# Kernel optimization log

Measured on AMD Instinct MI355X. Metric: run time of the kernel, lower is better.

## Reference

```python
import jax, jax.numpy as jnp
import numpy as np

TOP_K = 2
TEMPERATURE = 1.0


def setup_inputs() -> dict:
    key = jax.random.key(0)
    k1, k2, k3 = jax.random.split(key, 3)
    x = jax.random.normal(k1, (4, 2048, 2048), jnp.float32)
    # prototypes are top right-singular vectors of lora_A -> unit norm rows
    protos = jax.random.normal(k2, (8, 2048), jnp.float32)
    protos = protos / jnp.linalg.norm(protos, axis=-1, keepdims=True)
    # precomputed_W = stack of B @ A per expert, shape (E, out, in)
    W = jax.random.normal(k3, (8, 2048, 2048), jnp.float32) * 0.02
    return {"x": x, "prototypes": protos, "W": W, "scaling": 2}


def reference(x, prototypes, W, scaling):
    F_in = x.shape[-1]
    tok = x.reshape(-1, F_in)                      # (t, F)
    t = tok.shape[0]
    E = prototypes.shape[0]
    # Arrow routing: |<tok, proto_e>| similarity, keep top-k, softmax
    sim = jnp.abs(tok @ prototypes.T)              # (t, E)
    top_v, idx = jax.lax.top_k(sim, TOP_K)         # (t, k)
    neg_inf = jnp.asarray(-jnp.inf, tok.dtype)
    full_score = jnp.full((t, E), neg_inf, dtype=tok.dtype)
    full_score = full_score.at[jnp.arange(t)[:, None], idx].set(top_v)
    coeff = jax.nn.softmax(full_score / TEMPERATURE, axis=1)  # (t, E), zero off top-k
    # dense per-expert LoRA delta, then coefficient combine (as in source)
    W_tok = jnp.einsum('eoi,ti->eto', W, tok)      # (E, t, out)
    delta = jnp.einsum('te,eto->to', coeff, W_tok) # (t, out)
    delta = jnp.asarray(scaling, delta.dtype) * delta  # dropout = identity (eval)
    return delta.reshape(*x.shape[:-1], delta.shape[-1])
```

## Files before the change

kernel.cpp:

```cpp
#include <hip/hip_runtime.h>

#define T_TOK 8192
#define F_IN  2048
#define F_OUT 2048
#define N_EXP 8
#define NKS   (F_IN / 64)
#define MAXTILES 144
#define RT_TPB 16

typedef __attribute__((ext_vector_type(8))) short    short8;
typedef __attribute__((ext_vector_type(4))) float    f32x4;
typedef __attribute__((ext_vector_type(8))) _Float16 half8;
typedef unsigned short ushort;

#define AS1 __attribute__((address_space(1)))
#define AS3 __attribute__((address_space(3)))
#define GLOAD16(g, l) __builtin_amdgcn_global_load_lds((const AS1 unsigned int*)(g), \
                                                       (AS3 unsigned int*)(l), 16, 0, 0)

__device__ inline ushort f2bf(float f) {
    unsigned u = __float_as_uint(f);
    u += 0x7FFFu + ((u >> 16) & 1u);
    return (ushort)(u >> 16);
}

__global__ __launch_bounds__(256) void cvt_kernel(const float* __restrict__ in,
                                                  ushort* __restrict__ out, int n8) {
    for (int i = blockIdx.x * 256 + threadIdx.x; i < n8; i += gridDim.x * 256) {
        const float4 a = ((const float4*)in)[i * 2 + 0];
        const float4 b = ((const float4*)in)[i * 2 + 1];
        uint4 v;
        v.x = f2bf(a.x) | ((unsigned)f2bf(a.y) << 16);
        v.y = f2bf(a.z) | ((unsigned)f2bf(a.w) << 16);
        v.z = f2bf(b.x) | ((unsigned)f2bf(b.y) << 16);
        v.w = f2bf(b.z) | ((unsigned)f2bf(b.w) << 16);
        ((uint4*)out)[i] = v;
    }
}

__device__ inline void top2_store(const float* s, int ti, float sc,
                                  int* sh_ei, float (*sh_cf)[2]) {
    float v0 = -1.f; int i0 = 0;
    #pragma unroll
    for (int e = 0; e < N_EXP; ++e) {
        const float a = fabsf(s[e]);
        if (a > v0) { v0 = a; i0 = e; }
    }
    float v1 = -1.f; int i1 = 0;
    #pragma unroll
    for (int e = 0; e < N_EXP; ++e) {
        const float a = fabsf(s[e]);
        if (e != i0 && a > v1) { v1 = a; i1 = e; }
    }
    const float ex  = expf(v1 - v0);
    const float inv = 1.f / (1.f + ex);
    sh_ei[ti]    = i0 | (i1 << 16);
    sh_cf[ti][0] = sc * inv;
    sh_cf[ti][1] = sc * ex * inv;
}

__global__ __launch_bounds__(256) void route_kernel(
    const float* __restrict__ x, const float* __restrict__ protos,
    const int* __restrict__ scaling, ushort* __restrict__ xb,
    int* __restrict__ counts, int* __restrict__ lists, float* __restrict__ coeffs,
    int* __restrict__ pos)
{
    __shared__ int   sh_ei[RT_TPB];
    __shared__ float sh_cf[RT_TPB][2];
    __shared__ int   sh_base[N_EXP];

    const int wave = threadIdx.x >> 6;
    const int lane = threadIdx.x & 63;
    const float sc = (float)(*scaling);

    for (int pr = 0; pr < 2; ++pr) {
        const int ti0  = wave * 4 + pr * 2;
        const int tok0 = blockIdx.x * RT_TPB + ti0;
        const float* xr0 = x  + (size_t)tok0 * F_IN;
        const float* xr1 = xr0 + F_IN;
        ushort*      xo0 = xb + (size_t)tok0 * F_IN;
        ushort*      xo1 = xo0 + F_IN;

        float s0[N_EXP] = {}, s1[N_EXP] = {};
        for (int c = 0; c < F_IN / 256; ++c) {
            const int off = c * 256 + lane * 4;
            const float4 a = *(const float4*)(xr0 + off);
            const float4 b = *(const float4*)(xr1 + off);
            uint2 ba, bb;
            ba.x = f2bf(a.x) | ((unsigned)f2bf(a.y) << 16);
            ba.y = f2bf(a.z) | ((unsigned)f2bf(a.w) << 16);
            bb.x = f2bf(b.x) | ((unsigned)f2bf(b.y) << 16);
            bb.y = f2bf(b.z) | ((unsigned)f2bf(b.w) << 16);
            *(uint2*)(xo0 + off) = ba;
            *(uint2*)(xo1 + off) = bb;
            #pragma unroll
            for (int e = 0; e < N_EXP; ++e) {
                const float4 pv = *(const float4*)(protos + e * F_IN + off);
                s0[e] += a.x * pv.x + a.y * pv.y + a.z * pv.z + a.w * pv.w;
                s1[e] += b.x * pv.x + b.y * pv.y + b.z * pv.z + b.w * pv.w;
            }
        }
        #pragma unroll
        for (int e = 0; e < N_EXP; ++e) {
            float v0 = s0[e], v1 = s1[e];
            #pragma unroll
            for (int off = 32; off; off >>= 1) {
                v0 += __shfl_down(v0, off, 64);
                v1 += __shfl_down(v1, off, 64);
            }
            s0[e] = v0; s1[e] = v1;
        }
        if (lane == 0) {
            top2_store(s0, ti0,     sc, sh_ei, sh_cf);
            top2_store(s1, ti0 + 1, sc, sh_ei, sh_cf);
        }
    }
    __syncthreads();

    if (threadIdx.x < 64) {
        const int  p      = threadIdx.x;
        const bool active = p < RT_TPB * 2;
        const int  ti = p >> 1, j = p & 1;
        const int  e  = active ? ((sh_ei[ti] >> (j * 16)) & 0xffff) : 0xff;
        int rank = 0;
        #pragma unroll
        for (int ee = 0; ee < N_EXP; ++ee) {
            const unsigned long long m = __ballot(active && (e == ee));
            if (e == ee)
                rank = __popcll(m & ((1ull << p) - 1ull));
            if (p == ee && m != 0ull)
                sh_base[ee] = atomicAdd(&counts[ee], (int)__popcll(m));
        }
        if (active) {
            const int position = sh_base[e] + rank;
            const int gidx  = e * T_TOK + position;
            const int token = blockIdx.x * RT_TPB + ti;
            lists [gidx] = token;
            coeffs[gidx] = sh_cf[ti][j];
            pos[token * 2 + j] = gidx;
        }
    }
}

__global__ void plan_kernel(const int* __restrict__ counts, int* __restrict__ pbase,
                            int* __restrict__ ntiles, int* __restrict__ desc) {
    if (threadIdx.x == 0) {
        int pb = 0, t = 0;
        for (int e = 0; e < N_EXP; ++e) {
            pbase[e] = pb;
            const int ne = counts[e];
            const int nt = (ne + 127) >> 7;
            for (int i = 0; i < nt; ++i) desc[t++] = (e << 8) | i;
            pb += ne;
        }
        *ntiles = t;
    }
}

__global__ __launch_bounds__(256, 3) void gemm_kernel(
    const ushort* __restrict__ xb, const ushort* __restrict__ Wb,
    const int* __restrict__ counts, const int* __restrict__ lists,
    const int* __restrict__ pbase, const int* __restrict__ ntiles,
    const int* __restrict__ desc, _Float16* __restrict__ delta)
{
    if (blockIdx.x >= *ntiles) return;
    const int d     = desc[blockIdx.x];
    const int e     = d >> 8;
    const int tile  = d & 255;
    const int n_e   = counts[e];
    const int tbase = tile << 7;
    const int o0    = blockIdx.y * 128;
    const int prow0 = pbase[e] + tbase;

    __shared__ __align__(16) ushort As[128 * 64];
    __shared__ __align__(16) ushort Bs[128 * 64];

    const int tid  = threadIdx.x;
    const int lane = tid & 63;
    const int wid  = tid >> 6;
    const int wr   = wid >> 1, wc = wid & 1;

    const int ksrc = ((lane & 7) ^ (lane >> 3)) * 8;
    const ushort* srcA[4];
    const ushort* srcB[4];
    #pragma unroll
    for (int g = 0; g < 4; ++g) {
        const int row  = g * 32 + wid * 8 + (lane >> 3);
        const int slot = min(tbase + row, n_e - 1);
        srcA[g] = xb + (size_t)lists[e * T_TOK + slot] * F_IN + ksrc;
        srcB[g] = Wb + ((size_t)e * F_OUT + o0 + row) * F_IN + ksrc;
    }

    const int octx8 = ((lane >> 4) ^ (lane & 7)) * 8;
    const int ai    = (wr * 64 + (lane & 15)) * 64 + octx8;
    const int bi    = (wc * 64 + (lane & 15)) * 64 + octx8;

    f32x4 acc[4][4] = {};

    for (int ks = 0; ks < NKS; ++ks) {
        __syncthreads();
        #pragma unroll
        for (int g = 0; g < 4; ++g) {
            GLOAD16(srcA[g], As + (g * 32 + wid * 8) * 64);
            GLOAD16(srcB[g], Bs + (g * 32 + wid * 8) * 64);
            srcA[g] += 64; srcB[g] += 64;
        }
        __syncthreads();

        short8 a[4][2], b[4][2];
        #pragma unroll
        for (int m = 0; m < 4; ++m) {
            a[m][0] = *(const short8*)(As + (ai + m * 1024));
            a[m][1] = *(const short8*)(As + ((ai + m * 1024) ^ 32));
        }
        #pragma unroll
        for (int n = 0; n < 4; ++n) {
            b[n][0] = *(const short8*)(Bs + (bi + n * 1024));
            b[n][1] = *(const short8*)(Bs + ((bi + n * 1024) ^ 32));
        }
        #pragma unroll
        for (int kk = 0; kk < 2; ++kk)
            #pragma unroll
            for (int m = 0; m < 4; ++m)
                #pragma unroll
                for (int n = 0; n < 4; ++n)
                    acc[m][n] = __builtin_amdgcn_mfma_f32_16x16x32_bf16(
                        a[m][kk], b[n][kk], acc[m][n], 0, 0, 0);
    }

    const int rl = (lane >> 4) * 4;
    const int cl = lane & 15;
    #pragma unroll
    for (int m = 0; m < 4; ++m)
        #pragma unroll
        for (int rr = 0; rr < 4; ++rr) {
            const int srow = wr * 64 + m * 16 + rl + rr;
            if (tbase + srow < n_e) {
                _Float16* drow = delta + (size_t)(prow0 + srow) * F_OUT + o0 + wc * 64 + cl;
                #pragma unroll
                for (int n = 0; n < 4; ++n)
                    drow[n * 16] = (_Float16)acc[m][n][rr];
            }
        }
}

__global__ __launch_bounds__(256) void combine_kernel(
    const _Float16* __restrict__ delta, const int* __restrict__ pos,
    const float* __restrict__ coeffs, const int* __restrict__ pbase,
    float* __restrict__ out)
{
    const int tok = blockIdx.x;
    const int id0 = pos[tok * 2 + 0];
    const int id1 = pos[tok * 2 + 1];
    const float cf0 = coeffs[id0];
    const float cf1 = coeffs[id1];
    const int r0 = pbase[id0 >> 13] + (id0 & (T_TOK - 1));
    const int r1 = pbase[id1 >> 13] + (id1 & (T_TOK - 1));
    const int c  = threadIdx.x * 8;

    const half8 a = *(const half8*)(delta + (size_t)r0 * F_OUT + c);
    const half8 b = *(const half8*)(delta + (size_t)r1 * F_OUT + c);
    float4 o0, o1;
    o0.x = cf0 * (float)a[0] + cf1 * (float)b[0];
    o0.y = cf0 * (float)a[1] + cf1 * (float)b[1];
    o0.z = cf0 * (float)a[2] + cf1 * (float)b[2];
    o0.w = cf0 * (float)a[3] + cf1 * (float)b[3];
    o1.x = cf0 * (float)a[4] + cf1 * (float)b[4];
    o1.y = cf0 * (float)a[5] + cf1 * (float)b[5];
    o1.z = cf0 * (float)a[6] + cf1 * (float)b[6];
    o1.w = cf0 * (float)a[7] + cf1 * (float)b[7];
    float* op = out + (size_t)tok * F_OUT + c;
    *(float4*)(op)     = o0;
    *(float4*)(op + 4) = o1;
}

extern "C" void kernel_launch(void* const* d_in, const int* in_sizes, int n_in,
                              void* d_out, int out_size, void* d_ws, size_t ws_size,
                              hipStream_t stream) {
    const float* x      = (const float*)d_in[0];
    const float* protos = (const float*)d_in[1];
    const float* W      = (const float*)d_in[2];
    const int*   scal   = (const int*)d_in[3];
    float* out = (float*)d_out;

    char* ws = (char*)d_ws;
    int*      counts = (int*)(ws + 0);
    int*      pbase  = (int*)(ws + 64);
    int*      ntiles = (int*)(ws + 128);
    int*      desc   = (int*)(ws + 256);
    int*      pos    = (int*)(ws + 65536);
    int*      lists  = (int*)(ws + 262144);
    float*    coeffs = (float*)(ws + 524288);
    ushort*   xb     = (ushort*)(ws + (1ull << 20));
    ushort*   Wb     = (ushort*)(ws + (36ull << 20));
    _Float16* delta  = (_Float16*)(ws + (104ull << 20));

    hipMemsetAsync(counts, 0, N_EXP * sizeof(int), stream);

    cvt_kernel<<<2048, 256, 0, stream>>>(W, Wb, N_EXP * F_OUT * F_IN / 8);
    route_kernel<<<T_TOK / RT_TPB, 256, 0, stream>>>(x, protos, scal, xb, counts, lists, coeffs, pos);
    plan_kernel<<<1, 64, 0, stream>>>(counts, pbase, ntiles, desc);

    dim3 grid(MAXTILES, F_OUT / 128);
    gemm_kernel<<<grid, 256, 0, stream>>>(xb, Wb, counts, lists, pbase, ntiles, desc, delta);

    combine_kernel<<<T_TOK, 256, 0, stream>>>(delta, pos, coeffs, pbase, out);
}
```

Baseline: 339.1 us.

## Double-buffer LDS in routed GEMM with 128x256 tiles and XCD-aware block mapping

The grouped expert GEMM moves from 256-thread 128x128 tiles to 512-thread 128x256 tiles. Shared-memory A/B buffers are double-buffered so the global->LDS load for the next k-step is issued before the MFMAs on the current one, which drops one barrier per iteration. A 1D grid with a remap of the block index is meant to place neighbouring tiles on the same XCD for L2 reuse. The cost is more LDS per block (96KB) and an occupancy of one block per CU, so latency hiding depends on the prefetch.

```diff
diff --git a/kernel.cpp b/kernel.cpp
--- a/kernel.cpp
+++ b/kernel.cpp
@@ -157,39 +157,52 @@
     }
 }
 
-__global__ __launch_bounds__(256, 3) void gemm_kernel(
+__global__ __launch_bounds__(512, 1) void gemm_kernel(
     const ushort* __restrict__ xb, const ushort* __restrict__ Wb,
     const int* __restrict__ counts, const int* __restrict__ lists,
     const int* __restrict__ pbase, const int* __restrict__ ntiles,
     const int* __restrict__ desc, _Float16* __restrict__ delta)
 {
-    if (blockIdx.x >= *ntiles) return;
-    const int d     = desc[blockIdx.x];
+    const int hw = blockIdx.x;
+    const int l  = (hw & 7) * MAXTILES + (hw >> 3);
+    const int ti = l >> 3;
+    const int oi = l & 7;
+    if (ti >= *ntiles) return;
+
+    const int d     = desc[ti];
     const int e     = d >> 8;
     const int tile  = d & 255;
     const int n_e   = counts[e];
     const int tbase = tile << 7;
-    const int o0    = blockIdx.y * 128;
+    const int o0    = oi * 256;
     const int prow0 = pbase[e] + tbase;
 
-    __shared__ __align__(16) ushort As[128 * 64];
-    __shared__ __align__(16) ushort Bs[128 * 64];
+    __shared__ __align__(16) ushort Ald[2][128 * 64];
+    __shared__ __align__(16) ushort Bld[2][256 * 64];
 
     const int tid  = threadIdx.x;
     const int lane = tid & 63;
     const int wid  = tid >> 6;
-    const int wr   = wid >> 1, wc = wid & 1;
+    const int wr   = wid >> 2;
+    const int wc   = wid & 3;
 
     const int ksrc = ((lane & 7) ^ (lane >> 3)) * 8;
-    const ushort* srcA[4];
-    const ushort* srcB[4];
+    const ushort* srcA[2];
     #pragma unroll
-    for (int g = 0; g < 4; ++g) {
-        const int row  = g * 32 + wid * 8 + (lane >> 3);
+    for (int g = 0; g < 2; ++g) {
+        const int row  = g * 64 + wid * 8 + (lane >> 3);
         const int slot = min(tbase + row, n_e - 1);
         srcA[g] = xb + (size_t)lists[e * T_TOK + slot] * F_IN + ksrc;
-        srcB[g] = Wb + ((size_t)e * F_OUT + o0 + row) * F_IN + ksrc;
-    }
+    }
+    const ushort* srcB0 = Wb + ((size_t)(e * F_OUT + o0 + wid * 8 + (lane >> 3))) * F_IN + ksrc;
+
+    #define STAGE(BUF, KT) do { const size_t _k = (size_t)(KT) * 64;             \
+        ushort* _a = &Ald[BUF][0]; ushort* _b = &Bld[BUF][0];                    \
+        GLOAD16(srcA[0] + _k, _a + (wid * 8) * 64);                              \
+        GLOAD16(srcA[1] + _k, _a + (64 + wid * 8) * 64);                         \
+        _Pragma("unroll") for (int g = 0; g < 4; ++g)                            \
+            GLOAD16(srcB0 + (size_t)g * 64 * F_IN + _k, _b + (g * 64 + wid * 8) * 64); \
+    } while (0)
 
     const int octx8 = ((lane >> 4) ^ (lane & 7)) * 8;
     const int ai    = (wr * 64 + (lane & 15)) * 64 + octx8;
@@ -197,26 +210,25 @@
 
     f32x4 acc[4][4] = {};
 
+    STAGE(0, 0);
+    __syncthreads();
+
     for (int ks = 0; ks < NKS; ++ks) {
-        __syncthreads();
-        #pragma unroll
-        for (int g = 0; g < 4; ++g) {
-            GLOAD16(srcA[g], As + (g * 32 + wid * 8) * 64);
-            GLOAD16(srcB[g], Bs + (g * 32 + wid * 8) * 64);
-            srcA[g] += 64; srcB[g] += 64;
-        }
-        __syncthreads();
-
+        const int cur = ks & 1;
+        if (ks + 1 < NKS) STAGE(cur ^ 1, ks + 1);
+
+        const ushort* Ab = &Ald[cur][0];
+        const ushort* Bb = &Bld[cur][0];
         short8 a[4][2], b[4][2];
         #pragma unroll
         for (int m = 0; m < 4; ++m) {
-            a[m][0] = *(const short8*)(As + (ai + m * 1024));
-            a[m][1] = *(const short8*)(As + ((ai + m * 1024) ^ 32));
+            a[m][0] = *(const short8*)(Ab + (ai + m * 1024));
+            a[m][1] = *(const short8*)(Ab + ((ai + m * 1024) ^ 32));
         }
         #pragma unroll
         for (int n = 0; n < 4; ++n) {
-            b[n][0] = *(const short8*)(Bs + (bi + n * 1024));
-            b[n][1] = *(const short8*)(Bs + ((bi + n * 1024) ^ 32));
+            b[n][0] = *(const short8*)(Bb + (bi + n * 1024));
+            b[n][1] = *(const short8*)(Bb + ((bi + n * 1024) ^ 32));
         }
         #pragma unroll
         for (int kk = 0; kk < 2; ++kk)
@@ -226,6 +238,8 @@
                 for (int n = 0; n < 4; ++n)
                     acc[m][n] = __builtin_amdgcn_mfma_f32_16x16x32_bf16(
                         a[m][kk], b[n][kk], acc[m][n], 0, 0, 0);
+
+        __syncthreads();
     }
 
     const int rl = (lane >> 4) * 4;
@@ -301,8 +315,7 @@
     route_kernel<<<T_TOK / RT_TPB, 256, 0, stream>>>(x, protos, scal, xb, counts, lists, coeffs, pos);
     plan_kernel<<<1, 64, 0, stream>>>(counts, pbase, ntiles, desc);
 
-    dim3 grid(MAXTILES, F_OUT / 128);
-    gemm_kernel<<<grid, 256, 0, stream>>>(xb, Wb, counts, lists, pbase, ntiles, desc, delta);
+    gemm_kernel<<<MAXTILES * 8, 512, 0, stream>>>(xb, Wb, counts, lists, pbase, ntiles, desc, delta);
 
     combine_kernel<<<T_TOK, 256, 0, stream>>>(delta, pos, coeffs, pbase, out);
 }
```

Result: slower. 373.0 us (+10.0%).
